# Performance work log

Hardware: AMD Instinct MI355X
Metric: run time of the kernel (lower is better)

Reference implementation:

```python
import jax, jax.numpy as jnp
import numpy as np

N = 50000   # nodes
E = 800000  # edges
G = 128     # graphs in batch
H = 128     # hidden/out dim
K = 3       # GMM kernels
L = 4       # layers
PD = 2      # pseudo_dim_MoNet
NC = 10     # classes
BN_EPS = 1e-5


def setup_inputs() -> dict:
    key = jax.random.key(0)
    ks = jax.random.split(key, 16)
    s = 1.0 / np.sqrt(H)
    inp = {
        "feature": jax.random.normal(ks[0], (N, H), jnp.float32),
        "edge_index": jax.random.randint(ks[1], (2, E), 0, N, dtype=jnp.int32),
        "batch": jnp.sort(jax.random.randint(ks[2], (N,), 0, G, dtype=jnp.int32)),
        "emb_w": jax.random.normal(ks[3], (H, H), jnp.float32) * s,
        "emb_b": jnp.zeros((H,), jnp.float32),
        "fc_w": jax.random.normal(ks[4], (L, K * H, H), jnp.float32) * s,   # per-layer GMMConv fc (no bias)
        "mu": jax.random.normal(ks[5], (L, K, PD), jnp.float32) * 0.1,
        "inv_sigma": jnp.ones((L, K, PD), jnp.float32),
        "bn_gamma": jnp.ones((L, H), jnp.float32),
        "bn_beta": jnp.zeros((L, H), jnp.float32),
        "pp_w": jax.random.normal(ks[6], (L, PD, 2), jnp.float32) * 0.7,   # pseudo_proj Linear(2, dim)
        "pp_b": jnp.zeros((L, PD), jnp.float32),
        "mlp_w0": jax.random.normal(ks[7], (H // 2, H), jnp.float32) * s,
        "mlp_b0": jnp.zeros((H // 2,), jnp.float32),
        "mlp_w1": jax.random.normal(ks[8], (H // 4, H // 2), jnp.float32) * (1.0 / np.sqrt(H // 2)),
        "mlp_b1": jnp.zeros((H // 4,), jnp.float32),
        "mlp_w2": jax.random.normal(ks[9], (NC, H // 4), jnp.float32) * (1.0 / np.sqrt(H // 4)),
        "mlp_b2": jnp.zeros((NC,), jnp.float32),
    }
    return inp


def _forward(feature, edge_index, batch, emb_w, emb_b, fc_w, mu, inv_sigma,
             bn_gamma, bn_beta, pp_w, pp_b, mlp_w0, mlp_b0, mlp_w1, mlp_b1, mlp_w2, mlp_b2):
    row, col = edge_index[0], edge_index[1]
    h = feature @ emb_w.T + emb_b                                   # [N,H]

    # degree-based pseudo coordinates (per edge)
    ones_e = jnp.ones((E,), jnp.float32)
    deg_r = jax.ops.segment_sum(ones_e, row, num_segments=N)
    deg_c = jax.ops.segment_sum(ones_e, col, num_segments=N)
    srcs = 1.0 / jnp.sqrt(deg_r[row] + 1.0)
    dsts = 1.0 / jnp.sqrt(deg_c[col] + 1.0)
    pseudo = jnp.stack([srcs, dsts], axis=-1)                        # [E,2]

    for l in range(L):
        h_in = h
        ps = jnp.tanh(pseudo @ pp_w[l].T + pp_b[l])                  # [E,PD]
        # Gaussian mixture edge weights: exp(-0.5 * sum_d ((ps-mu)^2 * inv_sigma^2))
        diff = ps[:, None, :] - mu[l][None, :, :]                    # [E,K,PD]
        w = jnp.exp(-0.5 * jnp.sum(diff * diff * (inv_sigma[l] ** 2)[None], axis=-1))  # [E,K]
        h_src = h[row]                                               # [E,H] gather
        fcl = fc_w[l].reshape(K, H, H)
        msg = jnp.zeros((E, H), h.dtype)
        for k in range(K):                                           # small fixed K, avoids [E,K,H]
            msg = msg + w[:, k:k + 1] * (h_src @ fcl[k].T)
        agg = jax.ops.segment_sum(msg, col, num_segments=N)          # scatter-add to dst [N,H]
        # batch norm (batch statistics) + ReLU + residual; dropout=0 (identity)
        mean = jnp.mean(agg, axis=0)
        var = jnp.var(agg, axis=0)
        hn = (agg - mean) * jax.lax.rsqrt(var + BN_EPS) * bn_gamma[l] + bn_beta[l]
        h = h_in + jax.nn.relu(hn)

    # mean readout over graphs
    hs = jax.ops.segment_sum(h, batch, num_segments=G)               # [G,H]
    cnt = jax.ops.segment_sum(jnp.ones((N,), jnp.float32), batch, num_segments=G)
    hg = hs / jnp.maximum(cnt, 1.0)[:, None]

    z = jax.nn.relu(hg @ mlp_w0.T + mlp_b0)
    z = jax.nn.relu(z @ mlp_w1.T + mlp_b1)
    return z @ mlp_w2.T + mlp_b2                                     # [G,NC]


def reference(feature, edge_index, batch, emb_w, emb_b, fc_w, mu, inv_sigma,
              bn_gamma, bn_beta, pp_w, pp_b, mlp_w0, mlp_b0, mlp_w1, mlp_b1, mlp_w2, mlp_b2):
    return _forward(feature, edge_index, batch, emb_w, emb_b, fc_w, mu, inv_sigma,
                    bn_gamma, bn_beta, pp_w, pp_b, mlp_w0, mlp_b0, mlp_w1, mlp_b1, mlp_w2, mlp_b2)
```

## Files before the change

kernel.cpp:

```cpp
#include <hip/hip_runtime.h>
#include <hip/hip_bf16.h>

#define N_NODES 50000
#define N_EDGES 800000
#define N_GRAPHS 128
#define HID 128
#define NK 3
#define NL 4
#define NC 10
#define BN_EPS 1e-5f
#define SCAN_G ((N_NODES + 255) / 256)
#define NSLICE 32

#define BKT_SZ 8192
#define NBKT 7
#define FP_CHK 256
#define FP_E (N_EDGES / FP_CHK)

#define H_CHK 64
#define H_E (N_EDGES / H_CHK)
#define PKW (N_NODES / 2)

typedef __attribute__((ext_vector_type(8))) _Float16 half8;
typedef __attribute__((ext_vector_type(4))) float floatx4;
typedef __attribute__((ext_vector_type(2))) float float2v;
typedef __attribute__((ext_vector_type(2))) _Float16 half2v;
typedef __attribute__((ext_vector_type(4))) _Float16 half4v;

__device__ __forceinline__ float tanh_fast(float x) {
    float ax = fabsf(x);
    float t = __expf(-2.0f * ax);
    float r = (1.0f - t) / (1.0f + t);
    return copysignf(r, x);
}

__global__ __launch_bounds__(256) void hist_lds_kernel(const int* __restrict__ row,
                                                       const int* __restrict__ col,
                                                       unsigned* __restrict__ pr,
                                                       unsigned* __restrict__ pc) {
    __shared__ unsigned hh[PKW];
    int tid = threadIdx.x;
    const int4* arr = (const int4*)(blockIdx.y ? col : row);
    unsigned* out = (blockIdx.y ? pc : pr) + (size_t)blockIdx.x * PKW;
    uint4* hh4 = (uint4*)hh;
    const uint4 z4 = {0u, 0u, 0u, 0u};
    for (int i = tid; i < PKW / 4; i += 256) hh4[i] = z4;
    __syncthreads();
    int base4 = blockIdx.x * (H_E / 4);
    for (int i = tid; i < H_E / 4; i += 256) {
        int4 v = arr[base4 + i];
        atomicAdd(&hh[v.x >> 1], 1u << ((v.x & 1) << 4));
        atomicAdd(&hh[v.y >> 1], 1u << ((v.y & 1) << 4));
        atomicAdd(&hh[v.z >> 1], 1u << ((v.z & 1) << 4));
        atomicAdd(&hh[v.w >> 1], 1u << ((v.w & 1) << 4));
    }
    __syncthreads();
    uint4* out4 = (uint4*)out;
    for (int i = tid; i < PKW / 4; i += 256) out4[i] = hh4[i];
}

__global__ __launch_bounds__(256) void hist_reduce_kernel(const unsigned* __restrict__ pr,
                                                          const unsigned* __restrict__ pc,
                                                          int* __restrict__ degr,
                                                          int* __restrict__ degc) {
    int w = blockIdx.x * 256 + threadIdx.x;
    if (w >= PKW) return;
    unsigned rlo = 0, rhi = 0, clo = 0, chi = 0;
    for (int ch = 0; ch < H_CHK; ++ch) {
        unsigned a = pr[(size_t)ch * PKW + w];
        unsigned b = pc[(size_t)ch * PKW + w];
        rlo += a & 0xFFFFu; rhi += a >> 16;
        clo += b & 0xFFFFu; chi += b >> 16;
    }
    ((int2*)degr)[w] = make_int2((int)rlo, (int)rhi);
    ((int2*)degc)[w] = make_int2((int)clo, (int)chi);
}

__global__ __launch_bounds__(256) void scan1_kernel(const int* __restrict__ degc,
                                                    int* __restrict__ csr_off,
                                                    int* __restrict__ blocksum) {
    __shared__ int buf[256];
    int tid = threadIdx.x;
    int i = blockIdx.x * 256 + tid;
    int v = (i < N_NODES) ? degc[i] : 0;
    buf[tid] = v;
    __syncthreads();
    for (int d = 1; d < 256; d <<= 1) {
        int t = (tid >= d) ? buf[tid - d] : 0;
        __syncthreads();
        buf[tid] += t;
        __syncthreads();
    }
    if (i < N_NODES) csr_off[i] = buf[tid] - v;
    if (tid == 255) blocksum[blockIdx.x] = buf[255];
}

__global__ __launch_bounds__(256) void scan2_kernel(int* __restrict__ blocksum) {
    __shared__ int buf[256];
    int tid = threadIdx.x;
    int v = (tid < SCAN_G) ? blocksum[tid] : 0;
    buf[tid] = v;
    __syncthreads();
    for (int d = 1; d < 256; d <<= 1) {
        int t = (tid >= d) ? buf[tid - d] : 0;
        __syncthreads();
        buf[tid] += t;
        __syncthreads();
    }
    if (tid < SCAN_G) blocksum[tid] = buf[tid] - v;
}

__global__ __launch_bounds__(256) void scan3_kernel(const int* __restrict__ blocksum,
                                                    int* __restrict__ csr_off,
                                                    int* __restrict__ cursor) {
    int i = blockIdx.x * 256 + threadIdx.x;
    if (i < N_NODES) {
        int v = csr_off[i] + blocksum[blockIdx.x];
        csr_off[i] = v;
        cursor[i] = v;
    }
    if (i == 0) csr_off[N_NODES] = N_EDGES;
}

__global__ __launch_bounds__(256) void fill_src_kernel(const int* __restrict__ col,
                                                       const int* __restrict__ row,
                                                       int* __restrict__ cursor,
                                                       int* __restrict__ esrc) {
    int bkt = blockIdx.x & 7;
    if (bkt >= NBKT) return;
    int chunk = blockIdx.x >> 3;
    int base = bkt * BKT_SZ;
    int e0 = chunk * FP_E;
    for (int e = e0 + threadIdx.x; e < e0 + FP_E; e += 256) {
        unsigned c = (unsigned)(col[e] - base);
        if (c < BKT_SZ) {
            int pos = atomicAdd(&cursor[base + (int)c], 1);
            esrc[pos] = row[e];
        }
    }
}

__global__ void prep16_kernel(const float4* __restrict__ a, int n4a,
                              const float4* __restrict__ b, int n4b,
                              half4v* __restrict__ da, half4v* __restrict__ db,
                              const float* __restrict__ fc_w,
                              _Float16* __restrict__ w2t) {
    int i = blockIdx.x * blockDim.x + threadIdx.x;
    if (i < n4a + n4b) {
        const float4* src; half4v* dst; int idx;
        if (i < n4a) { src = a; dst = da; idx = i; }
        else { src = b; dst = db; idx = i - n4a; }
        float4 f = src[idx];
        half4v o;
        o.x = (_Float16)f.x; o.y = (_Float16)f.y; o.z = (_Float16)f.z; o.w = (_Float16)f.w;
        dst[idx] = o;
        return;
    }
    int idx = i - (n4a + n4b);
    if (idx >= NL * NK * HID * HID) return;
    int ii = idx & (HID - 1);
    int j = (idx >> 7) & (HID - 1);
    int kl = idx >> 14;
    int k = kl % 3;
    int l = kl / 3;
    w2t[((size_t)(l * HID + j)) * (NK * HID) + k * HID + ii] = (_Float16)fc_w[idx];
}

__global__ __launch_bounds__(256) void gemm_f16_kernel(
        const _Float16* __restrict__ A, const _Float16* __restrict__ W,
        const float* __restrict__ bias, _Float16* __restrict__ C16,
        float* __restrict__ bnsum, int M, int Kd) {
    __shared__ _Float16 sA[64 * 40], sB[128 * 40];
    __shared__ float bsum[HID], bsq[HID];
    int tid = threadIdx.x;
    if (bnsum && tid < HID) { bsum[tid] = 0.f; bsq[tid] = 0.f; }
    int bm = blockIdx.x * 64;
    int wave = tid >> 6, lane = tid & 63;
    int ln = lane & 15, quad = lane >> 4;
    int wy = wave >> 1, wx = wave & 1;
    int srow = tid >> 2, scol = (tid & 3) << 3;
    floatx4 acc[2][4] = {};
    const half8 zv = {0, 0, 0, 0, 0, 0, 0, 0};

    half8 pA, pB[2];
    bool av0 = (bm + srow) < M;
    const size_t aoff0 = (size_t)(bm + srow) * Kd + scol;
    const size_t woff0 = (size_t)srow * Kd + scol;
    const size_t woff1 = (size_t)(srow + 64) * Kd + scol;

#define LOAD_TILE(K0)                                                          \
    do {                                                                       \
        pB[0] = *(const half8*)(W + woff0 + (K0));                             \
        pB[1] = *(const half8*)(W + woff1 + (K0));                             \
        pA = av0 ? *(const half8*)(A + aoff0 + (K0)) : zv;                     \
    } while (0)

    LOAD_TILE(0);
    for (int k0 = 0; k0 < Kd; k0 += 32) {
        __syncthreads();
        *(half8*)&sA[srow * 40 + scol] = pA;
        *(half8*)&sB[srow * 40 + scol] = pB[0];
        *(half8*)&sB[(srow + 64) * 40 + scol] = pB[1];
        __syncthreads();
        if (k0 + 32 < Kd) LOAD_TILE(k0 + 32);
        half8 a[2], b[4];
        int kq = quad * 8;
#pragma unroll
        for (int i = 0; i < 2; ++i)
            a[i] = *(const half8*)&sA[(wy * 32 + i * 16 + ln) * 40 + kq];
#pragma unroll
        for (int j = 0; j < 4; ++j)
            b[j] = *(const half8*)&sB[(wx * 64 + j * 16 + ln) * 40 + kq];
#pragma unroll
        for (int i = 0; i < 2; ++i)
#pragma unroll
            for (int j = 0; j < 4; ++j)
                acc[i][j] = __builtin_amdgcn_mfma_f32_16x16x32_f16(a[i], b[j], acc[i][j], 0, 0, 0);
    }
#undef LOAD_TILE

#pragma unroll
    for (int j = 0; j < 4; ++j) {
        int gc = wx * 64 + j * 16 + ln;
        float bv = bias ? bias[gc] : 0.f;
#pragma unroll
        for (int i = 0; i < 2; ++i) {
#pragma unroll
            for (int r = 0; r < 4; ++r) {
                int gr = bm + wy * 32 + i * 16 + quad * 4 + r;
                if (gr < M) C16[(size_t)gr * HID + gc] = (_Float16)(acc[i][j][r] + bv);
            }
        }
    }
    if (bnsum) {
#pragma unroll
        for (int j = 0; j < 4; ++j) {
            float s = 0.f, q = 0.f;
#pragma unroll
            for (int i = 0; i < 2; ++i)
#pragma unroll
                for (int r = 0; r < 4; ++r) { float v = acc[i][j][r]; s += v; q += v * v; }
            s += __shfl_xor(s, 16); s += __shfl_xor(s, 32);
            q += __shfl_xor(q, 16); q += __shfl_xor(q, 32);
            if (quad == 0) {
                atomicAdd(&bsum[wx * 64 + j * 16 + ln], s);
                atomicAdd(&bsq[wx * 64 + j * 16 + ln], q);
            }
        }
        __syncthreads();
        float* slice = bnsum + (blockIdx.x & (NSLICE - 1)) * (2 * HID);
        if (tid < HID) {
            atomicAdd(&slice[tid],       bsum[tid]);
            atomicAdd(&slice[HID + tid], bsq[tid]);
        }
    }
}

__global__ __launch_bounds__(128) void bn_finalize_kernel(const float* __restrict__ slices,
                                                          const float* __restrict__ gamma,
                                                          const float* __restrict__ beta,
                                                          float* __restrict__ sc_sh) {
    int t = threadIdx.x;
    float s = 0.f, q = 0.f;
    for (int sl = 0; sl < NSLICE; ++sl) {
        s += slices[sl * (2 * HID) + t];
        q += slices[sl * (2 * HID) + HID + t];
    }
    const float invN = 1.0f / (float)N_NODES;
    float mean = s * invN;
    float var = q * invN - mean * mean;
    float scale = gamma[t] * rsqrtf(var + BN_EPS);
    sc_sh[t] = scale;
    sc_sh[HID + t] = beta[t] - mean * scale;
}

__global__ __launch_bounds__(256) void aggregate_kernel(const int* __restrict__ csr_off,
                                                        const int* __restrict__ esrc,
                                                        const int* __restrict__ degr,
                                                        const int* __restrict__ degc,
                                                        const char* __restrict__ h16,
                                                        _Float16* __restrict__ u,
                                                        const float* __restrict__ pw,
                                                        const float* __restrict__ pb,
                                                        const float* __restrict__ mu,
                                                        const float* __restrict__ isg) {
    int wave = threadIdx.x >> 6;
    int lane = threadIdx.x & 63;
    int sub = lane >> 5;
    int sl = lane & 31;
    int base = sub << 5;
    int n = blockIdx.x * 8 + wave * 2 + sub;
    if (n >= N_NODES) return;
    int beg = csr_off[n], end = csr_off[n + 1];
    float py = rsqrtf((float)degc[n] + 1.0f);
    float pw0 = pw[0], pw1 = pw[1], pw2 = pw[2], pw3 = pw[3];
    float pb0 = pb[0], pb1 = pb[1];
    float m00 = mu[0], m01 = mu[1], m10 = mu[2], m11 = mu[3], m20 = mu[4], m21 = mu[5];
    float s00 = isg[0], s01 = isg[1], s10 = isg[2], s11 = isg[3], s20 = isg[4], s21 = isg[5];
    const char* hb = h16 + sl * 8;
    floatx4 a0 = {0.f, 0.f, 0.f, 0.f}, a1 = a0, a2 = a0;

    for (int chunk = beg; chunk < end; chunk += 32) {
        int ce = chunk + sl;
        int rsrc = (ce < end) ? esrc[ce] : 0;
        float px = rsqrtf((float)degr[rsrc] + 1.0f);
        int roff = rsrc << 8;
        float ps0 = tanh_fast(px * pw0 + py * pw1 + pb0);
        float ps1 = tanh_fast(px * pw2 + py * pw3 + pb1);
        float d0 = ps0 - m00, d1 = ps1 - m01;
        float w0 = __expf(-0.5f * (d0 * d0 * s00 * s00 + d1 * d1 * s01 * s01));
        d0 = ps0 - m10; d1 = ps1 - m11;
        float w1 = __expf(-0.5f * (d0 * d0 * s10 * s10 + d1 * d1 * s11 * s11));
        d0 = ps0 - m20; d1 = ps1 - m21;
        float w2 = __expf(-0.5f * (d0 * d0 * s20 * s20 + d1 * d1 * s21 * s21));
        int m = end - chunk; if (m > 32) m = 32;
        int t = 0;
        for (; t + 8 <= m; t += 8) {
            int ro[8];
#pragma unroll
            for (int s = 0; s < 8; ++s) ro[s] = __shfl(roff, base + t + s);
            half4v hv[8];
#pragma unroll
            for (int s = 0; s < 8; ++s) hv[s] = *(const half4v*)(hb + (unsigned)ro[s]);
#pragma unroll
            for (int s = 0; s < 8; ++s) {
                float wx = __shfl(w0, base + t + s);
                float wy = __shfl(w1, base + t + s);
                float wz = __shfl(w2, base + t + s);
                floatx4 hf = {(float)hv[s].x, (float)hv[s].y, (float)hv[s].z, (float)hv[s].w};
                a0 += wx * hf;
                a1 += wy * hf;
                a2 += wz * hf;
            }
        }
        for (; t < m; ++t) {
            int ro = __shfl(roff, base + t);
            float wx = __shfl(w0, base + t);
            float wy = __shfl(w1, base + t);
            float wz = __shfl(w2, base + t);
            half4v hv = *(const half4v*)(hb + (unsigned)ro);
            floatx4 hf = {(float)hv.x, (float)hv.y, (float)hv.z, (float)hv.w};
            a0 += wx * hf;
            a1 += wy * hf;
            a2 += wz * hf;
        }
    }
    size_t b = (size_t)n * 384 + sl * 4;
    half4v o0, o1, o2;
    o0.x = (_Float16)a0.x; o0.y = (_Float16)a0.y; o0.z = (_Float16)a0.z; o0.w = (_Float16)a0.w;
    o1.x = (_Float16)a1.x; o1.y = (_Float16)a1.y; o1.z = (_Float16)a1.z; o1.w = (_Float16)a1.w;
    o2.x = (_Float16)a2.x; o2.y = (_Float16)a2.y; o2.z = (_Float16)a2.z; o2.w = (_Float16)a2.w;
    *(half4v*)(u + b)       = o0;
    *(half4v*)(u + b + 128) = o1;
    *(half4v*)(u + b + 256) = o2;
}

__global__ void bn_apply_kernel(half4v* __restrict__ h16,
                                const half4v* __restrict__ agg16,
                                const float* __restrict__ sc_sh) {
    int idx = blockIdx.x * blockDim.x + threadIdx.x;
    if (idx >= N_NODES * HID / 4) return;
    int c = (idx & 31) * 4;
    half4v a = agg16[idx];
    half4v hv = h16[idx];
    half4v o16;
#pragma unroll
    for (int j = 0; j < 4; ++j) {
        float hn = (float)a[j] * sc_sh[c + j] + sc_sh[HID + c + j];
        o16[j] = (_Float16)((float)hv[j] + fmaxf(hn, 0.f));
    }
    h16[idx] = o16;
}

__global__ __launch_bounds__(1024) void readout_mlp_kernel(const _Float16* __restrict__ h16,
                                                           const int* __restrict__ batch,
                                                           const float* __restrict__ w0, const float* __restrict__ b0,
                                                           const float* __restrict__ w1, const float* __restrict__ b1,
                                                           const float* __restrict__ w2, const float* __restrict__ b2,
                                                           float* __restrict__ out) {
    __shared__ float part[8][128];
    __shared__ float hg[128];
    __shared__ float z0[64];
    __shared__ float z1[32];
    __shared__ int range[2];
    int g = blockIdx.x;
    int tid = threadIdx.x;
    if (tid == 0) {
        int lo = 0, hi = N_NODES;
        while (lo < hi) { int mid = (lo + hi) >> 1; if (batch[mid] < g) lo = mid + 1; else hi = mid; }
        range[0] = lo;
        hi = N_NODES;
        while (lo < hi) { int mid = (lo + hi) >> 1; if (batch[mid] < g + 1) lo = mid + 1; else hi = mid; }
        range[1] = lo;
    }
    __syncthreads();
    int lo = range[0], hi = range[1];
    int rg = tid >> 7;
    int ch = tid & 127;
    float s0 = 0.f, s1 = 0.f, s2 = 0.f, s3 = 0.f;
    int n = lo + rg;
    for (; n + 24 < hi; n += 32) {
        s0 += (float)h16[(size_t)n * HID + ch];
        s1 += (float)h16[(size_t)(n + 8) * HID + ch];
        s2 += (float)h16[(size_t)(n + 16) * HID + ch];
        s3 += (float)h16[(size_t)(n + 24) * HID + ch];
    }
    for (; n < hi; n += 8) s0 += (float)h16[(size_t)n * HID + ch];
    part[rg][ch] = (s0 + s1) + (s2 + s3);
    __syncthreads();
    if (tid < 128) {
        float s = 0.f;
#pragma unroll
        for (int r = 0; r < 8; ++r) s += part[r][tid];
        int cnt = hi - lo; if (cnt < 1) cnt = 1;
        hg[tid] = s / (float)cnt;
    }
    __syncthreads();
    if (tid < 64) {
        float a = b0[tid];
        for (int i = 0; i < 128; ++i) a += hg[i] * w0[tid * 128 + i];
        z0[tid] = fmaxf(a, 0.f);
    }
    __syncthreads();
    if (tid < 32) {
        float a = b1[tid];
        for (int i = 0; i < 64; ++i) a += z0[i] * w1[tid * 64 + i];
        z1[tid] = fmaxf(a, 0.f);
    }
    __syncthreads();
    if (tid < 10) {
        float a = b2[tid];
        for (int i = 0; i < 32; ++i) a += z1[i] * w2[tid * 32 + i];
        out[g * NC + tid] = a;
    }
}

extern "C" void kernel_launch(void* const* d_in, const int* in_sizes, int n_in,
                              void* d_out, int out_size, void* d_ws, size_t ws_size,
                              hipStream_t stream) {
    const float* feature = (const float*)d_in[0];
    const int*   edge    = (const int*)d_in[1];
    const int*   row     = edge;
    const int*   col     = edge + N_EDGES;
    const int*   batch   = (const int*)d_in[2];
    const float* emb_w   = (const float*)d_in[3];
    const float* emb_b   = (const float*)d_in[4];
    const float* fc_w    = (const float*)d_in[5];
    const float* mu      = (const float*)d_in[6];
    const float* isig    = (const float*)d_in[7];
    const float* gamma   = (const float*)d_in[8];
    const float* beta    = (const float*)d_in[9];
    const float* pp_w    = (const float*)d_in[10];
    const float* pp_b    = (const float*)d_in[11];
    const float* mw0     = (const float*)d_in[12];
    const float* mb0     = (const float*)d_in[13];
    const float* mw1     = (const float*)d_in[14];
    const float* mb1     = (const float*)d_in[15];
    const float* mw2     = (const float*)d_in[16];
    const float* mb2     = (const float*)d_in[17];
    float* out = (float*)d_out;

    char* ws = (char*)d_ws;
    size_t off = 0;
    auto carve = [&](size_t bytes) { size_t o = off; off = (off + bytes + 255) & ~(size_t)255; return o; };
    _Float16* h16   = (_Float16*)(ws + carve((size_t)N_NODES * HID * 2));
    _Float16* u     = (_Float16*)(ws + carve((size_t)N_NODES * NK * HID * 2));
    _Float16* agg16 = (_Float16*)(ws + carve((size_t)N_NODES * HID * 2));
    int* esrc       = (int*)(ws + carve((size_t)N_EDGES * 4));
    _Float16* w2t   = (_Float16*)(ws + carve((size_t)NL * HID * NK * HID * 2));
    _Float16* f16   = (_Float16*)(ws + carve((size_t)N_NODES * HID * 2));
    _Float16* e16   = (_Float16*)(ws + carve((size_t)HID * HID * 2));
    int* degr       = (int*)(ws + carve((size_t)N_NODES * 4));
    int* degc       = (int*)(ws + carve((size_t)N_NODES * 4));
    int* csr_off    = (int*)(ws + carve((size_t)(N_NODES + 1) * 4));
    int* cursor     = (int*)(ws + carve((size_t)N_NODES * 4));
    int* blocksum   = (int*)(ws + carve((size_t)SCAN_G * 4));
    unsigned* pr    = (unsigned*)(ws + carve((size_t)H_CHK * PKW * 4));
    unsigned* pc    = (unsigned*)(ws + carve((size_t)H_CHK * PKW * 4));
    float* bnsum    = (float*)(ws + carve((size_t)NL * NSLICE * 2 * HID * 4));
    float* bnfin    = (float*)(ws + carve((size_t)NL * 2 * HID * 4));
    (void)ws_size; (void)in_sizes; (void)n_in; (void)out_size;

    hipMemsetAsync(bnsum, 0, (size_t)NL * NSLICE * 2 * HID * 4, stream);

    hist_lds_kernel<<<dim3(H_CHK, 2), 256, 0, stream>>>(row, col, pr, pc);
    hist_reduce_kernel<<<(PKW + 255) / 256, 256, 0, stream>>>(pr, pc, degr, degc);
    scan1_kernel<<<SCAN_G, 256, 0, stream>>>(degc, csr_off, blocksum);
    scan2_kernel<<<1, 256, 0, stream>>>(blocksum);
    scan3_kernel<<<SCAN_G, 256, 0, stream>>>(blocksum, csr_off, cursor);
    fill_src_kernel<<<FP_CHK * 8, 256, 0, stream>>>(col, row, cursor, esrc);

    prep16_kernel<<<((N_NODES * HID + HID * HID) / 4 + NL * NK * HID * HID + 255) / 256,
                    256, 0, stream>>>(
        (const float4*)feature, N_NODES * HID / 4, (const float4*)emb_w, HID * HID / 4,
        (half4v*)f16, (half4v*)e16, fc_w, w2t);

    gemm_f16_kernel<<<(N_NODES + 63) / 64, 256, 0, stream>>>(
        f16, e16, emb_b, h16, nullptr, N_NODES, HID);

    for (int l = 0; l < NL; ++l) {
        aggregate_kernel<<<(N_NODES + 7) / 8, 256, 0, stream>>>(
            csr_off, esrc, degr, degc, (const char*)h16, u,
            pp_w + l * 4, pp_b + l * 2, mu + l * 6, isig + l * 6);
        gemm_f16_kernel<<<(N_NODES + 63) / 64, 256, 0, stream>>>(
            u, w2t + (size_t)l * HID * NK * HID, nullptr, agg16,
            bnsum + (size_t)l * NSLICE * 2 * HID, N_NODES, NK * HID);
        bn_finalize_kernel<<<1, 128, 0, stream>>>(
            bnsum + (size_t)l * NSLICE * 2 * HID, gamma + l * HID, beta + l * HID,
            bnfin + l * 2 * HID);
        bn_apply_kernel<<<(N_NODES * HID / 4 + 255) / 256, 256, 0, stream>>>(
            (half4v*)h16, (const half4v*)agg16, bnfin + l * 2 * HID);
    }

    readout_mlp_kernel<<<N_GRAPHS, 1024, 0, stream>>>(h16, batch, mw0, mb0, mw1, mb1, mw2, mb2, out);
}
```

Baseline: 452.4 us.

## Fuse edge aggregation with per-layer GMM GEMM through shared memory

Merges the aggregation kernel and the per-layer 384-wide GEMM into one kernel. Each block aggregates 32 nodes into an LDS tile, then runs MFMA against the layer weights and accumulates batch-norm statistics. This removes the global write and read of the N×384 fp16 intermediate and one launch per layer. The cost is fewer rows per GEMM block, so each block reloads the weight tile more often, plus higher LDS use that may lower occupancy.

```diff
diff --git a/kernel.cpp b/kernel.cpp
--- a/kernel.cpp
+++ b/kernel.cpp
@@ -20,6 +20,9 @@
 #define H_CHK 64
 #define H_E (N_EDGES / H_CHK)
 #define PKW (N_NODES / 2)
+
+#define AG_BM 32
+#define UA_STRIDE 392
 
 typedef __attribute__((ext_vector_type(8))) _Float16 half8;
 typedef __attribute__((ext_vector_type(4))) float floatx4;
@@ -169,11 +172,9 @@
 __global__ __launch_bounds__(256) void gemm_f16_kernel(
         const _Float16* __restrict__ A, const _Float16* __restrict__ W,
         const float* __restrict__ bias, _Float16* __restrict__ C16,
-        float* __restrict__ bnsum, int M, int Kd) {
+        int M, int Kd) {
     __shared__ _Float16 sA[64 * 40], sB[128 * 40];
-    __shared__ float bsum[HID], bsq[HID];
     int tid = threadIdx.x;
-    if (bnsum && tid < HID) { bsum[tid] = 0.f; bsq[tid] = 0.f; }
     int bm = blockIdx.x * 64;
     int wave = tid >> 6, lane = tid & 63;
     int ln = lane & 15, quad = lane >> 4;
@@ -230,28 +231,6 @@
                 int gr = bm + wy * 32 + i * 16 + quad * 4 + r;
                 if (gr < M) C16[(size_t)gr * HID + gc] = (_Float16)(acc[i][j][r] + bv);
             }
-        }
-    }
-    if (bnsum) {
-#pragma unroll
-        for (int j = 0; j < 4; ++j) {
-            float s = 0.f, q = 0.f;
-#pragma unroll
-            for (int i = 0; i < 2; ++i)
-#pragma unroll
-                for (int r = 0; r < 4; ++r) { float v = acc[i][j][r]; s += v; q += v * v; }
-            s += __shfl_xor(s, 16); s += __shfl_xor(s, 32);
-            q += __shfl_xor(q, 16); q += __shfl_xor(q, 32);
-            if (quad == 0) {
-                atomicAdd(&bsum[wx * 64 + j * 16 + ln], s);
-                atomicAdd(&bsq[wx * 64 + j * 16 + ln], q);
-            }
-        }
-        __syncthreads();
-        float* slice = bnsum + (blockIdx.x & (NSLICE - 1)) * (2 * HID);
-        if (tid < HID) {
-            atomicAdd(&slice[tid],       bsum[tid]);
-            atomicAdd(&slice[HID + tid], bsq[tid]);
         }
     }
 }
@@ -274,85 +253,149 @@
     sc_sh[HID + t] = beta[t] - mean * scale;
 }
 
-__global__ __launch_bounds__(256) void aggregate_kernel(const int* __restrict__ csr_off,
-                                                        const int* __restrict__ esrc,
-                                                        const int* __restrict__ degr,
-                                                        const int* __restrict__ degc,
-                                                        const char* __restrict__ h16,
-                                                        _Float16* __restrict__ u,
-                                                        const float* __restrict__ pw,
-                                                        const float* __restrict__ pb,
-                                                        const float* __restrict__ mu,
-                                                        const float* __restrict__ isg) {
-    int wave = threadIdx.x >> 6;
-    int lane = threadIdx.x & 63;
+__global__ __launch_bounds__(256) void agg_gemm_kernel(
+        const int* __restrict__ csr_off, const int* __restrict__ esrc,
+        const int* __restrict__ degr, const int* __restrict__ degc,
+        const char* __restrict__ h16, const _Float16* __restrict__ W,
+        _Float16* __restrict__ C16, float* __restrict__ bnsum,
+        const float* __restrict__ pw, const float* __restrict__ pb,
+        const float* __restrict__ mu, const float* __restrict__ isg) {
+    __shared__ _Float16 uA[AG_BM * UA_STRIDE];
+    __shared__ _Float16 sB[128 * 40];
+    __shared__ float bsum[HID], bsq[HID];
+    int tid = threadIdx.x;
+    if (tid < HID) { bsum[tid] = 0.f; bsq[tid] = 0.f; }
+    int wave = tid >> 6, lane = tid & 63;
     int sub = lane >> 5;
     int sl = lane & 31;
     int base = sub << 5;
-    int n = blockIdx.x * 8 + wave * 2 + sub;
-    if (n >= N_NODES) return;
-    int beg = csr_off[n], end = csr_off[n + 1];
-    float py = rsqrtf((float)degc[n] + 1.0f);
+    int bm = blockIdx.x * AG_BM;
+
     float pw0 = pw[0], pw1 = pw[1], pw2 = pw[2], pw3 = pw[3];
     float pb0 = pb[0], pb1 = pb[1];
     float m00 = mu[0], m01 = mu[1], m10 = mu[2], m11 = mu[3], m20 = mu[4], m21 = mu[5];
     float s00 = isg[0], s01 = isg[1], s10 = isg[2], s11 = isg[3], s20 = isg[4], s21 = isg[5];
     const char* hb = h16 + sl * 8;
-    floatx4 a0 = {0.f, 0.f, 0.f, 0.f}, a1 = a0, a2 = a0;
-
-    for (int chunk = beg; chunk < end; chunk += 32) {
-        int ce = chunk + sl;
-        int rsrc = (ce < end) ? esrc[ce] : 0;
-        float px = rsqrtf((float)degr[rsrc] + 1.0f);
-        int roff = rsrc << 8;
-        float ps0 = tanh_fast(px * pw0 + py * pw1 + pb0);
-        float ps1 = tanh_fast(px * pw2 + py * pw3 + pb1);
-        float d0 = ps0 - m00, d1 = ps1 - m01;
-        float w0 = __expf(-0.5f * (d0 * d0 * s00 * s00 + d1 * d1 * s01 * s01));
-        d0 = ps0 - m10; d1 = ps1 - m11;
-        float w1 = __expf(-0.5f * (d0 * d0 * s10 * s10 + d1 * d1 * s11 * s11));
-        d0 = ps0 - m20; d1 = ps1 - m21;
-        float w2 = __expf(-0.5f * (d0 * d0 * s20 * s20 + d1 * d1 * s21 * s21));
-        int m = end - chunk; if (m > 32) m = 32;
-        int t = 0;
-        for (; t + 8 <= m; t += 8) {
-            int ro[8];
-#pragma unroll
-            for (int s = 0; s < 8; ++s) ro[s] = __shfl(roff, base + t + s);
-            half4v hv[8];
-#pragma unroll
-            for (int s = 0; s < 8; ++s) hv[s] = *(const half4v*)(hb + (unsigned)ro[s]);
-#pragma unroll
-            for (int s = 0; s < 8; ++s) {
-                float wx = __shfl(w0, base + t + s);
-                float wy = __shfl(w1, base + t + s);
-                float wz = __shfl(w2, base + t + s);
-                floatx4 hf = {(float)hv[s].x, (float)hv[s].y, (float)hv[s].z, (float)hv[s].w};
-                a0 += wx * hf;
-                a1 += wy * hf;
-                a2 += wz * hf;
+
+#pragma unroll 1
+    for (int pass = 0; pass < 4; ++pass) {
+        int lnode = pass * 8 + wave * 2 + sub;
+        int n = bm + lnode;
+        floatx4 a0 = {0.f, 0.f, 0.f, 0.f}, a1 = a0, a2 = a0;
+        if (n < N_NODES) {
+            int beg = csr_off[n], end = csr_off[n + 1];
+            float py = rsqrtf((float)degc[n] + 1.0f);
+            for (int chunk = beg; chunk < end; chunk += 32) {
+                int ce = chunk + sl;
+                int rsrc = (ce < end) ? esrc[ce] : 0;
+                float px = rsqrtf((float)degr[rsrc] + 1.0f);
+                int roff = rsrc << 8;
+                float ps0 = tanh_fast(px * pw0 + py * pw1 + pb0);
+                float ps1 = tanh_fast(px * pw2 + py * pw3 + pb1);
+                float d0 = ps0 - m00, d1 = ps1 - m01;
+                float w0 = __expf(-0.5f * (d0 * d0 * s00 * s00 + d1 * d1 * s01 * s01));
+                d0 = ps0 - m10; d1 = ps1 - m11;
+                float w1 = __expf(-0.5f * (d0 * d0 * s10 * s10 + d1 * d1 * s11 * s11));
+                d0 = ps0 - m20; d1 = ps1 - m21;
+                float w2 = __expf(-0.5f * (d0 * d0 * s20 * s20 + d1 * d1 * s21 * s21));
+                int m = end - chunk; if (m > 32) m = 32;
+                int t = 0;
+                for (; t + 8 <= m; t += 8) {
+                    int ro[8];
+#pragma unroll
+                    for (int s = 0; s < 8; ++s) ro[s] = __shfl(roff, base + t + s);
+                    half4v hv[8];
+#pragma unroll
+                    for (int s = 0; s < 8; ++s) hv[s] = *(const half4v*)(hb + (unsigned)ro[s]);
+#pragma unroll
+                    for (int s = 0; s < 8; ++s) {
+                        float wx = __shfl(w0, base + t + s);
+                        float wy = __shfl(w1, base + t + s);
+                        float wz = __shfl(w2, base + t + s);
+                        floatx4 hf = {(float)hv[s].x, (float)hv[s].y, (float)hv[s].z, (float)hv[s].w};
+                        a0 += wx * hf;
+                        a1 += wy * hf;
+                        a2 += wz * hf;
+                    }
+                }
+                for (; t < m; ++t) {
+                    int ro = __shfl(roff, base + t);
+                    float wx = __shfl(w0, base + t);
+                    float wy = __shfl(w1, base + t);
+                    float wz = __shfl(w2, base + t);
+                    half4v hv = *(const half4v*)(hb + (unsigned)ro);
+                    floatx4 hf = {(float)hv.x, (float)hv.y, (float)hv.z, (float)hv.w};
+                    a0 += wx * hf;
+                    a1 += wy * hf;
+                    a2 += wz * hf;
+                }
             }
         }
-        for (; t < m; ++t) {
-            int ro = __shfl(roff, base + t);
-            float wx = __shfl(w0, base + t);
-            float wy = __shfl(w1, base + t);
-            float wz = __shfl(w2, base + t);
-            half4v hv = *(const half4v*)(hb + (unsigned)ro);
-            floatx4 hf = {(float)hv.x, (float)hv.y, (float)hv.z, (float)hv.w};
-            a0 += wx * hf;
-            a1 += wy * hf;
-            a2 += wz * hf;
+        _Float16* urow = &uA[lnode * UA_STRIDE + sl * 4];
+        half4v o0, o1, o2;
+        o0.x = (_Float16)a0.x; o0.y = (_Float16)a0.y; o0.z = (_Float16)a0.z; o0.w = (_Float16)a0.w;
+        o1.x = (_Float16)a1.x; o1.y = (_Float16)a1.y; o1.z = (_Float16)a1.z; o1.w = (_Float16)a1.w;
+        o2.x = (_Float16)a2.x; o2.y = (_Float16)a2.y; o2.z = (_Float16)a2.z; o2.w = (_Float16)a2.w;
+        *(half4v*)(urow)       = o0;
+        *(half4v*)(urow + 128) = o1;
+        *(half4v*)(urow + 256) = o2;
+    }
+
+    int ln = lane & 15, quad = lane >> 4;
+    int wy = wave >> 1, wx = wave & 1;
+    int srow = tid >> 2, scol = (tid & 3) << 3;
+    floatx4 acc[4] = {};
+    const size_t woff0 = (size_t)srow * (NK * HID) + scol;
+    const size_t woff1 = (size_t)(srow + 64) * (NK * HID) + scol;
+    half8 pB0 = *(const half8*)(W + woff0);
+    half8 pB1 = *(const half8*)(W + woff1);
+    for (int k0 = 0; k0 < NK * HID; k0 += 32) {
+        __syncthreads();
+        *(half8*)&sB[srow * 40 + scol] = pB0;
+        *(half8*)&sB[(srow + 64) * 40 + scol] = pB1;
+        __syncthreads();
+        if (k0 + 32 < NK * HID) {
+            pB0 = *(const half8*)(W + woff0 + k0 + 32);
+            pB1 = *(const half8*)(W + woff1 + k0 + 32);
         }
-    }
-    size_t b = (size_t)n * 384 + sl * 4;
-    half4v o0, o1, o2;
-    o0.x = (_Float16)a0.x; o0.y = (_Float16)a0.y; o0.z = (_Float16)a0.z; o0.w = (_Float16)a0.w;
-    o1.x = (_Float16)a1.x; o1.y = (_Float16)a1.y; o1.z = (_Float16)a1.z; o1.w = (_Float16)a1.w;
-    o2.x = (_Float16)a2.x; o2.y = (_Float16)a2.y; o2.z = (_Float16)a2.z; o2.w = (_Float16)a2.w;
-    *(half4v*)(u + b)       = o0;
-    *(half4v*)(u + b + 128) = o1;
-    *(half4v*)(u + b + 256) = o2;
+        int kq = quad * 8;
+        half8 a = *(const half8*)&uA[(wy * 16 + ln) * UA_STRIDE + k0 + kq];
+        half8 b[4];
+#pragma unroll
+        for (int j = 0; j < 4; ++j)
+            b[j] = *(const half8*)&sB[(wx * 64 + j * 16 + ln) * 40 + kq];
+#pragma unroll
+        for (int j = 0; j < 4; ++j)
+            acc[j] = __builtin_amdgcn_mfma_f32_16x16x32_f16(a, b[j], acc[j], 0, 0, 0);
+    }
+
+#pragma unroll
+    for (int j = 0; j < 4; ++j) {
+        int gc = wx * 64 + j * 16 + ln;
+#pragma unroll
+        for (int r = 0; r < 4; ++r) {
+            int gr = bm + wy * 16 + quad * 4 + r;
+            if (gr < N_NODES) C16[(size_t)gr * HID + gc] = (_Float16)acc[j][r];
+        }
+    }
+#pragma unroll
+    for (int j = 0; j < 4; ++j) {
+        float s = 0.f, q = 0.f;
+#pragma unroll
+        for (int r = 0; r < 4; ++r) { float v = acc[j][r]; s += v; q += v * v; }
+        s += __shfl_xor(s, 16); s += __shfl_xor(s, 32);
+        q += __shfl_xor(q, 16); q += __shfl_xor(q, 32);
+        if (quad == 0) {
+            atomicAdd(&bsum[wx * 64 + j * 16 + ln], s);
+            atomicAdd(&bsq[wx * 64 + j * 16 + ln], q);
+        }
+    }
+    __syncthreads();
+    float* slice = bnsum + (blockIdx.x & (NSLICE - 1)) * (2 * HID);
+    if (tid < HID) {
+        atomicAdd(&slice[tid],       bsum[tid]);
+        atomicAdd(&slice[HID + tid], bsq[tid]);
+    }
 }
 
 __global__ void bn_apply_kernel(half4v* __restrict__ h16,
@@ -464,7 +507,6 @@
     size_t off = 0;
     auto carve = [&](size_t bytes) { size_t o = off; off = (off + bytes + 255) & ~(size_t)255; return o; };
     _Float16* h16   = (_Float16*)(ws + carve((size_t)N_NODES * HID * 2));
-    _Float16* u     = (_Float16*)(ws + carve((size_t)N_NODES * NK * HID * 2));
     _Float16* agg16 = (_Float16*)(ws + carve((size_t)N_NODES * HID * 2));
     int* esrc       = (int*)(ws + carve((size_t)N_EDGES * 4));
     _Float16* w2t   = (_Float16*)(ws + carve((size_t)NL * HID * NK * HID * 2));
@@ -496,15 +538,14 @@
         (half4v*)f16, (half4v*)e16, fc_w, w2t);
 
     gemm_f16_kernel<<<(N_NODES + 63) / 64, 256, 0, stream>>>(
-        f16, e16, emb_b, h16, nullptr, N_NODES, HID);
+        f16, e16, emb_b, h16, N_NODES, HID);
 
     for (int l = 0; l < NL; ++l) {
-        aggregate_kernel<<<(N_NODES + 7) / 8, 256, 0, stream>>>(
-            csr_off, esrc, degr, degc, (const char*)h16, u,
+        agg_gemm_kernel<<<(N_NODES + AG_BM - 1) / AG_BM, 256, 0, stream>>>(
+            csr_off, esrc, degr, degc, (const char*)h16,
+            w2t + (size_t)l * HID * NK * HID, agg16,
+            bnsum + (size_t)l * NSLICE * 2 * HID,
             pp_w + l * 4, pp_b + l * 2, mu + l * 6, isig + l * 6);
-        gemm_f16_kernel<<<(N_NODES + 63) / 64, 256, 0, stream>>>(
-            u, w2t + (size_t)l * HID * NK * HID, nullptr, agg16,
-            bnsum + (size_t)l * NSLICE * 2 * HID, N_NODES, NK * HID);
         bn_finalize_kernel<<<1, 128, 0, stream>>>(
             bnsum + (size_t)l * NSLICE * 2 * HID, gamma + l * HID, beta + l * HID,
             bnfin + l * 2 * HID);
```

New measurement: 538.1 us. +18.9%, slower.
